# Performance work log

Hardware: AMD Instinct MI355X
Metric: run time of the kernel (lower is better)

The kernel has to match this reference:

```python
import jax, jax.numpy as jnp
import numpy as np

DIM = 1024
NUM_HEADS = 16
HEAD_DIM = DIM // NUM_HEADS
SCALE = HEAD_DIM ** -0.5


def setup_inputs() -> dict:
    key = jax.random.key(0)
    k1, k2, k3 = jax.random.split(key, 3)
    B, N = 2, 2048
    x = jax.random.normal(k1, (B, N, DIM), dtype=jnp.float32)
    W_qkv = jax.random.normal(k2, (DIM, 3 * DIM), dtype=jnp.float32) * (DIM ** -0.5)
    b_qkv = jnp.zeros((3 * DIM,), dtype=jnp.float32)
    W_proj = jax.random.normal(k3, (DIM, DIM), dtype=jnp.float32) * (DIM ** -0.5)
    b_proj = jnp.zeros((DIM,), dtype=jnp.float32)
    return {"x": x, "W_qkv": W_qkv, "b_qkv": b_qkv, "W_proj": W_proj, "b_proj": b_proj}


def reference(x, W_qkv, b_qkv, W_proj, b_proj):
    B, N, D = x.shape
    qkv = x @ W_qkv + b_qkv                      # [B, N, 3D]
    qkv = qkv.reshape(B, N, 3, NUM_HEADS, HEAD_DIM)
    qkv = jnp.transpose(qkv, (2, 0, 3, 1, 4))    # [3, B, H, N, hd]
    q, k, v = qkv[0], qkv[1], qkv[2]
    attn = jnp.einsum('bhqd,bhkd->bhqk', q, k) * SCALE  # [B, H, N, N]
    attn = jax.nn.softmax(attn, axis=-1)
    out = jnp.einsum('bhqk,bhkd->bhqd', attn, v)        # [B, H, N, hd]
    out = jnp.transpose(out, (0, 2, 1, 3)).reshape(B, N, D)
    out = out @ W_proj + b_proj
    return out
```

## Files before the change

kernel.cpp:

```cpp
#include <hip/hip_runtime.h>


typedef __bf16 bf16_t;
typedef __bf16 bf16x2 __attribute__((ext_vector_type(2)));
typedef __bf16 bf16x4 __attribute__((ext_vector_type(4)));
typedef __bf16 bf16x8 __attribute__((ext_vector_type(8)));
typedef float  f32x4  __attribute__((ext_vector_type(4)));

#define NTOK 2048
#define DIM  1024
#define NH   16
#define HD   64
#define SCL2 0.18033688011112042f

#define MFMA16(a, b, c) __builtin_amdgcn_mfma_f32_16x16x32_bf16((a), (b), (c), 0, 0, 0)

__device__ __forceinline__ void gload_lds16(const void* g, void* l) {
  __builtin_amdgcn_global_load_lds((const __attribute__((address_space(1))) void*)g,
                                   (__attribute__((address_space(3))) void*)l, 16, 0, 0);
}

__device__ __forceinline__ void transpose_cvt_tile(const float* __restrict__ W,
                                                   bf16_t* __restrict__ WT,
                                                   int rows, int cols, int bx, int by) {
  __shared__ float tile[32][33];
  int j0 = bx * 32, i0 = by * 32;
  int c = threadIdx.x & 31, r0 = threadIdx.x >> 5;
#pragma unroll
  for (int it = 0; it < 4; ++it) {
    int r = r0 + it * 8;
    tile[r][c] = W[(long)(i0 + r) * cols + j0 + c];
  }
  __syncthreads();
#pragma unroll
  for (int it = 0; it < 4; ++it) {
    int r = r0 + it * 8;
    WT[(long)(j0 + r) * rows + i0 + c] = (bf16_t)tile[c][r];
  }
}

__global__ __launch_bounds__(256) void k_prep(const float* __restrict__ x,
                                              bf16_t* __restrict__ xb,
                                              const float* __restrict__ Wq,
                                              bf16_t* __restrict__ WqT,
                                              const float* __restrict__ Wp,
                                              bf16_t* __restrict__ WpT) {
  int id = blockIdx.x;
  if (id < 2048) {
    int i = (id * 256 + threadIdx.x) * 8;
    float4 a = *(const float4*)(x + i);
    float4 b = *(const float4*)(x + i + 4);
    bf16x8 v;
    v[0] = (bf16_t)a.x; v[1] = (bf16_t)a.y; v[2] = (bf16_t)a.z; v[3] = (bf16_t)a.w;
    v[4] = (bf16_t)b.x; v[5] = (bf16_t)b.y; v[6] = (bf16_t)b.z; v[7] = (bf16_t)b.w;
    *(bf16x8*)(xb + i) = v;
  } else if (id < 2048 + 3072) {
    int t = id - 2048;
    transpose_cvt_tile(Wq, WqT, 1024, 3072, t % 96, t / 96);
  } else {
    int t = id - 5120;
    transpose_cvt_tile(Wp, WpT, 1024, 1024, t & 31, t >> 5);
  }
}

__device__ __forceinline__ void gemm_core(const bf16_t* __restrict__ A,
                                          const bf16_t* __restrict__ B,
                                          int K, int bm, int bn,
                                          bf16_t* As, bf16_t* Bs, f32x4 acc[4][4]) {
  const int t = threadIdx.x;
  const int lane = t & 63;
  const int w = t >> 6;
  const int wr = (w >> 1) * 64, wc = (w & 1) * 64;
  const int l15 = lane & 15, g = lane >> 4;
  const int srow = t >> 2, scol = (t & 3) * 8;
  const f32x4 vzero = {0.f, 0.f, 0.f, 0.f};
#pragma unroll
  for (int m = 0; m < 4; ++m)
#pragma unroll
    for (int n = 0; n < 4; ++n) acc[m][n] = vzero;

  const bf16_t* ga = A + (long)(bm + srow) * K + scol;
  const bf16_t* gb = B + (long)(bn + srow) * K + scol;
  bf16_t* lA = As + srow * 32 + scol;
  bf16_t* lB = Bs + srow * 32 + scol;
  const long rstep = 64l * K;

  for (int k0 = 0; k0 < K; k0 += 32) {
    gload_lds16(ga + k0,         lA);
    gload_lds16(ga + rstep + k0, lA + 64 * 32);
    gload_lds16(gb + k0,         lB);
    gload_lds16(gb + rstep + k0, lB + 64 * 32);
    __syncthreads();
    bf16x8 af[4], bfv[4];
#pragma unroll
    for (int m = 0; m < 4; ++m)
      af[m] = *(const bf16x8*)(As + (wr + m * 16 + l15) * 32 + g * 8);
#pragma unroll
    for (int n = 0; n < 4; ++n)
      bfv[n] = *(const bf16x8*)(Bs + (wc + n * 16 + l15) * 32 + g * 8);
#pragma unroll
    for (int m = 0; m < 4; ++m)
#pragma unroll
      for (int n = 0; n < 4; ++n)
        acc[m][n] = MFMA16(af[m], bfv[n], acc[m][n]);
    __syncthreads();
  }
}

__global__ __launch_bounds__(256) void k_gemm_qkv(const bf16_t* __restrict__ xb,
                                                  const bf16_t* __restrict__ WqT,
                                                  const float* __restrict__ bq,
                                                  bf16_t* __restrict__ Qb,
                                                  bf16_t* __restrict__ Kb,
                                                  bf16_t* __restrict__ Vt) {
  __shared__ alignas(16) bf16_t As[128 * 32];
  __shared__ alignas(16) bf16_t Bs[128 * 32];
  f32x4 acc[4][4];
  const int bm = blockIdx.y * 128, bn = blockIdx.x * 128;
  gemm_core(xb, WqT, DIM, bm, bn, As, Bs, acc);

  const int lane = threadIdx.x & 63, w = threadIdx.x >> 6;
  const int wr = (w >> 1) * 64, wc = (w & 1) * 64;
  const int l15 = lane & 15, g = lane >> 4;
#pragma unroll
  for (int n = 0; n < 4; ++n) {
    int col = bn + wc + n * 16 + l15;
    float bias = bq[col];
    int t3 = col >> 10, rem = col & 1023;
    int h = rem >> 6, d = rem & 63;
#pragma unroll
    for (int m = 0; m < 4; ++m) {
      int rowb = bm + wr + m * 16 + g * 4;
#pragma unroll
      for (int r = 0; r < 4; ++r) {
        int row = rowb + r;
        int b = row >> 11, tok = row & 2047;
        int bh = b * NH + h;
        float val = acc[m][n][r] + bias;
        if (t3 == 0)      Qb[bh * (NTOK * HD) + tok * HD + d] = (bf16_t)(val * SCL2);
        else if (t3 == 1) Kb[bh * (NTOK * HD) + tok * HD + d] = (bf16_t)val;
        else              Vt[bh * (NTOK * HD) + d * NTOK + tok] = (bf16_t)val;
      }
    }
  }
}

__global__ __launch_bounds__(256, 4) void k_attn(const bf16_t* __restrict__ Qb,
                                                 const bf16_t* __restrict__ Kb,
                                                 const bf16_t* __restrict__ Vt,
                                                 bf16_t* __restrict__ Ob) {
  __shared__ alignas(16) bf16_t Ks[2][64 * 64];
  __shared__ alignas(16) bf16_t Vs[2][64 * 64];
  __shared__ alignas(16) char  P2[4][2048];

  const int b0 = blockIdx.x;
  const int swz = (b0 & 7) * 128 + (b0 >> 3);
  const int qt = swz & 31, bh = swz >> 5;
  const int b = bh >> 4, h = bh & 15;
  const int t = threadIdx.x;
  const int w = t >> 6, lane = t & 63;
  const int l15 = lane & 15, g = lane >> 4;
  const bf16_t* Qp = Qb + bh * (NTOK * HD);
  const bf16_t* Kp = Kb + bh * (NTOK * HD);
  const bf16_t* Vp = Vt + bh * (NTOK * HD);
  const int q0 = qt * 64 + w * 16;
  char* P2w = &P2[w][0];

  const int sr = t >> 2, sc0 = (t & 3) * 2;
  const bf16_t* gK = Kp + sr * HD + sc0 * 8;
  const bf16_t* gV = Vp + (long)sr * NTOK + sc0 * 8;
  const int lko0 = sr * 128 + ((sc0 ^ (sr & 7)) << 4);
  const int cs0 = ((g ^ (l15 & 7)) << 4);
  const int cs1 = cs0 ^ 64;

  bf16x8 qfr[2];
#pragma unroll
  for (int kk = 0; kk < 2; ++kk)
    qfr[kk] = *(const bf16x8*)(Qp + (q0 + l15) * HD + kk * 32 + g * 8);

  bf16x8 ones;
#pragma unroll
  for (int i = 0; i < 8; ++i) ones[i] = (bf16_t)1.0f;

  const f32x4 vzero = {0.f, 0.f, 0.f, 0.f};
  f32x4 o[4];
#pragma unroll
  for (int df = 0; df < 4; ++df) o[df] = vzero;
  f32x4 o_sum = vzero;

  bf16x8 kst0, kst1, vst0, vst1;
  kst0 = *(const bf16x8*)(gK);
  kst1 = *(const bf16x8*)(gK + 8);
  vst0 = *(const bf16x8*)(gV);
  vst1 = *(const bf16x8*)(gV + 8);
  *(bf16x8*)((char*)Ks[0] + lko0)        = kst0;
  *(bf16x8*)((char*)Ks[0] + (lko0 ^ 16)) = kst1;
  *(bf16x8*)((char*)Vs[0] + lko0)        = vst0;
  *(bf16x8*)((char*)Vs[0] + (lko0 ^ 16)) = vst1;
  __syncthreads();
  int cur = 0;

  for (int kt = 0; kt < NTOK; kt += 64) {
    const bool more = (kt + 64) < NTOK;
    if (more) {
      kst0 = *(const bf16x8*)(gK + (kt + 64) * HD);
      kst1 = *(const bf16x8*)(gK + (kt + 64) * HD + 8);
      vst0 = *(const bf16x8*)(gV + (kt + 64));
      vst1 = *(const bf16x8*)(gV + (kt + 64) + 8);
    }
    const char* kbuf = (const char*)Ks[cur];
    const char* vbuf = (const char*)Vs[cur];
    f32x4 s[4];
    __builtin_amdgcn_s_setprio(1);
#pragma unroll
    for (int kf = 0; kf < 4; ++kf) {
      int rb = (kf * 16 + l15) * 128;
      bf16x8 ka0 = *(const bf16x8*)(kbuf + rb + cs0);
      bf16x8 ka1 = *(const bf16x8*)(kbuf + rb + cs1);
      s[kf] = MFMA16(ka0, qfr[0], vzero);
      s[kf] = MFMA16(ka1, qfr[1], s[kf]);
    }
    __builtin_amdgcn_s_setprio(0);
#pragma unroll
    for (int kf = 0; kf < 4; ++kf) {
      bf16x4 pw;
      pw[0] = (bf16_t)__builtin_amdgcn_exp2f(s[kf][0]);
      pw[1] = (bf16_t)__builtin_amdgcn_exp2f(s[kf][1]);
      pw[2] = (bf16_t)__builtin_amdgcn_exp2f(s[kf][2]);
      pw[3] = (bf16_t)__builtin_amdgcn_exp2f(s[kf][3]);
      *(bf16x4*)(P2w + (2 * kf + (g >> 1)) * 256 + l15 * 16 + 8 * (g & 1)) = pw;
    }
    __builtin_amdgcn_s_setprio(1);
#pragma unroll
    for (int kb = 0; kb < 2; ++kb) {
      bf16x8 pf = *(const bf16x8*)(P2w + kb * 1024 + lane * 16);
      int csk = kb ? cs1 : cs0;
      o_sum = MFMA16(ones, pf, o_sum);
#pragma unroll
      for (int df = 0; df < 4; ++df) {
        bf16x8 va = *(const bf16x8*)(vbuf + (df * 16 + l15) * 128 + csk);
        o[df] = MFMA16(va, pf, o[df]);
      }
    }
    __builtin_amdgcn_s_setprio(0);
    if (more) {
      *(bf16x8*)((char*)Ks[cur ^ 1] + lko0)        = kst0;
      *(bf16x8*)((char*)Ks[cur ^ 1] + (lko0 ^ 16)) = kst1;
      *(bf16x8*)((char*)Vs[cur ^ 1] + lko0)        = vst0;
      *(bf16x8*)((char*)Vs[cur ^ 1] + (lko0 ^ 16)) = vst1;
    }
    __syncthreads();
    cur ^= 1;
  }
  float inv = 1.0f / o_sum[0];
  int tok = q0 + l15;
  bf16_t* op = Ob + (long)(b * NTOK + tok) * DIM + h * HD;
#pragma unroll
  for (int df = 0; df < 4; ++df) {
#pragma unroll
    for (int rp = 0; rp < 2; ++rp) {
      bf16x2 v2;
      v2[0] = (bf16_t)(o[df][rp * 2]     * inv);
      v2[1] = (bf16_t)(o[df][rp * 2 + 1] * inv);
      *(bf16x2*)(op + df * 16 + g * 4 + rp * 2) = v2;
    }
  }
}

__global__ __launch_bounds__(256) void k_gemm_proj(const bf16_t* __restrict__ Ob,
                                                   const bf16_t* __restrict__ WpT,
                                                   const float* __restrict__ bp,
                                                   float* __restrict__ out) {
  __shared__ alignas(16) bf16_t As[128 * 32];
  __shared__ alignas(16) bf16_t Bs[128 * 32];
  f32x4 acc[4][4];
  const int bm = blockIdx.y * 128, bn = blockIdx.x * 128;
  gemm_core(Ob, WpT, DIM, bm, bn, As, Bs, acc);

  const int lane = threadIdx.x & 63, w = threadIdx.x >> 6;
  const int wr = (w >> 1) * 64, wc = (w & 1) * 64;
  const int l15 = lane & 15, g = lane >> 4;
#pragma unroll
  for (int n = 0; n < 4; ++n) {
    int col = bn + wc + n * 16 + l15;
    float bias = bp[col];
#pragma unroll
    for (int m = 0; m < 4; ++m) {
      int rowb = bm + wr + m * 16 + g * 4;
#pragma unroll
      for (int r = 0; r < 4; ++r)
        out[(long)(rowb + r) * DIM + col] = acc[m][n][r] + bias;
    }
  }
}

extern "C" void kernel_launch(void* const* d_in, const int* in_sizes, int n_in,
                              void* d_out, int out_size, void* d_ws, size_t ws_size,
                              hipStream_t stream) {
  const float* x     = (const float*)d_in[0];
  const float* Wqkv  = (const float*)d_in[1];
  const float* bqkv  = (const float*)d_in[2];
  const float* Wproj = (const float*)d_in[3];
  const float* bproj = (const float*)d_in[4];
  float* out = (float*)d_out;

  char* ws = (char*)d_ws;
  bf16_t* xb  = (bf16_t*)(ws);
  bf16_t* WqT = (bf16_t*)(ws + (8l  << 20));
  bf16_t* WpT = (bf16_t*)(ws + (14l << 20));
  bf16_t* Qb  = (bf16_t*)(ws + (16l << 20));
  bf16_t* Kb  = (bf16_t*)(ws + (24l << 20));
  bf16_t* Vt  = (bf16_t*)(ws + (32l << 20));
  bf16_t* Ob  = (bf16_t*)(ws);

  k_prep<<<6144, 256, 0, stream>>>(x, xb, Wqkv, WqT, Wproj, WpT);
  k_gemm_qkv<<<dim3(24, 32), 256, 0, stream>>>(xb, WqT, bqkv, Qb, Kb, Vt);
  k_attn<<<1024, 256, 0, stream>>>(Qb, Kb, Vt, Ob);
  k_gemm_proj<<<dim3(8, 32), 256, 0, stream>>>(Ob, WpT, bproj, out);
}
```

Measured before the change: 130.5 us.

## Pre-swizzle K/V tiles in QKV epilogue and stage via direct global-to-LDS loads

The QKV GEMM epilogue now writes K and V (transposed) in a 64-token-tiled layout that already carries the LDS XOR swizzle. The attention kernel can then copy each tile contiguously with global_load_lds, skipping the register staging and the separate LDS stores. This frees registers and VALU/LDS-store slots and lets the next tile's loads overlap compute. The risk is that the async LDS loads must finish before the barrier; the code relies on __syncthreads to wait for the outstanding vmcnt.

```diff
diff --git a/kernel.cpp b/kernel.cpp
--- a/kernel.cpp
+++ b/kernel.cpp
@@ -137,9 +137,19 @@
         int b = row >> 11, tok = row & 2047;
         int bh = b * NH + h;
         float val = acc[m][n][r] + bias;
-        if (t3 == 0)      Qb[bh * (NTOK * HD) + tok * HD + d] = (bf16_t)(val * SCL2);
-        else if (t3 == 1) Kb[bh * (NTOK * HD) + tok * HD + d] = (bf16_t)val;
-        else              Vt[bh * (NTOK * HD) + d * NTOK + tok] = (bf16_t)val;
+        if (t3 == 0) {
+          Qb[bh * (NTOK * HD) + tok * HD + d] = (bf16_t)(val * SCL2);
+        } else if (t3 == 1) {
+          int rr = tok & 63;
+          int off = bh * (NTOK * HD) + (tok >> 6) * 4096 + rr * 64 +
+                    (((d >> 3) ^ (rr & 7)) << 3) + (d & 7);
+          Kb[off] = (bf16_t)val;
+        } else {
+          int ct = tok & 63;
+          int off = bh * (NTOK * HD) + (tok >> 6) * 4096 + d * 64 +
+                    (((ct >> 3) ^ (d & 7)) << 3) + (ct & 7);
+          Vt[off] = (bf16_t)val;
+        }
       }
     }
   }
@@ -166,10 +176,6 @@
   const int q0 = qt * 64 + w * 16;
   char* P2w = &P2[w][0];
 
-  const int sr = t >> 2, sc0 = (t & 3) * 2;
-  const bf16_t* gK = Kp + sr * HD + sc0 * 8;
-  const bf16_t* gV = Vp + (long)sr * NTOK + sc0 * 8;
-  const int lko0 = sr * 128 + ((sc0 ^ (sr & 7)) << 4);
   const int cs0 = ((g ^ (l15 & 7)) << 4);
   const int cs1 = cs0 ^ 64;
 
@@ -188,26 +194,21 @@
   for (int df = 0; df < 4; ++df) o[df] = vzero;
   f32x4 o_sum = vzero;
 
-  bf16x8 kst0, kst1, vst0, vst1;
-  kst0 = *(const bf16x8*)(gK);
-  kst1 = *(const bf16x8*)(gK + 8);
-  vst0 = *(const bf16x8*)(gV);
-  vst1 = *(const bf16x8*)(gV + 8);
-  *(bf16x8*)((char*)Ks[0] + lko0)        = kst0;
-  *(bf16x8*)((char*)Ks[0] + (lko0 ^ 16)) = kst1;
-  *(bf16x8*)((char*)Vs[0] + lko0)        = vst0;
-  *(bf16x8*)((char*)Vs[0] + (lko0 ^ 16)) = vst1;
+  auto stage = [&](int buf, int tile) {
+    const bf16_t* gk = Kp + tile * 4096 + t * 8;
+    const bf16_t* gv = Vp + tile * 4096 + t * 8;
+    gload_lds16(gk,        (char*)Ks[buf] + t * 16);
+    gload_lds16(gk + 2048, (char*)Ks[buf] + 4096 + t * 16);
+    gload_lds16(gv,        (char*)Vs[buf] + t * 16);
+    gload_lds16(gv + 2048, (char*)Vs[buf] + 4096 + t * 16);
+  };
+
+  stage(0, 0);
   __syncthreads();
   int cur = 0;
 
   for (int kt = 0; kt < NTOK; kt += 64) {
-    const bool more = (kt + 64) < NTOK;
-    if (more) {
-      kst0 = *(const bf16x8*)(gK + (kt + 64) * HD);
-      kst1 = *(const bf16x8*)(gK + (kt + 64) * HD + 8);
-      vst0 = *(const bf16x8*)(gV + (kt + 64));
-      vst1 = *(const bf16x8*)(gV + (kt + 64) + 8);
-    }
+    if (kt + 64 < NTOK) stage(cur ^ 1, (kt >> 6) + 1);
     const char* kbuf = (const char*)Ks[cur];
     const char* vbuf = (const char*)Vs[cur];
     f32x4 s[4];
@@ -243,12 +244,6 @@
       }
     }
     __builtin_amdgcn_s_setprio(0);
-    if (more) {
-      *(bf16x8*)((char*)Ks[cur ^ 1] + lko0)        = kst0;
-      *(bf16x8*)((char*)Ks[cur ^ 1] + (lko0 ^ 16)) = kst1;
-      *(bf16x8*)((char*)Vs[cur ^ 1] + lko0)        = vst0;
-      *(bf16x8*)((char*)Vs[cur ^ 1] + (lko0 ^ 16)) = vst1;
-    }
     __syncthreads();
     cur ^= 1;
   }
```

Result: faster. 125.7 us (-3.7%).
